# Kernel optimization log

Measured on AMD Instinct MI355X. Metric: run time of the kernel, lower is better.

Reference implementation:

```python
import jax, jax.numpy as jnp
import numpy as np

N = 50000      # nodes
E = 1600000    # edges
F_IN = 128     # input_dim
H = 160        # hidden_dim
G = 512        # graphs in batch
C = 2          # num_classes
EPS = 1e-5     # BatchNorm eps


def setup_inputs() -> dict:
    key = jax.random.key(0)
    ks = jax.random.split(key, 12)
    x = jax.random.normal(ks[0], (N, F_IN), jnp.float32)
    edge_index = jax.random.randint(ks[1], (2, E), 0, N, dtype=jnp.int32)
    batch = jnp.sort(jax.random.randint(ks[2], (N,), 0, G, dtype=jnp.int32))

    def lin(k, fi, fo):
        s = 1.0 / np.sqrt(fi)
        kw, kb = jax.random.split(k)
        W = jax.random.uniform(kw, (fi, fo), jnp.float32, -s, s)
        b = jax.random.uniform(kb, (fo,), jnp.float32, -s, s)
        return W, b

    W1, b1 = lin(ks[3], F_IN, H)
    W2, b2 = lin(ks[4], H, H)
    W3, b3 = lin(ks[5], H, H)
    Wc1, bc1 = lin(ks[6], H, H // 2)
    Wc2, bc2 = lin(ks[7], H // 2, C)

    def bn(k):
        k1, k2, k3, k4 = jax.random.split(k, 4)
        gamma = jax.random.uniform(k1, (H,), jnp.float32, 0.5, 1.5)
        beta = jax.random.normal(k2, (H,), jnp.float32) * 0.1
        mean = jax.random.normal(k3, (H,), jnp.float32) * 0.1
        var = jax.random.uniform(k4, (H,), jnp.float32, 0.5, 1.5)
        return gamma, beta, mean, var

    g1, be1, m1, v1 = bn(ks[8])
    g2, be2, m2, v2 = bn(ks[9])
    g3, be3, m3, v3 = bn(ks[10])

    return dict(x=x, edge_index=edge_index, batch=batch,
                W1=W1, b1=b1, W2=W2, b2=b2, W3=W3, b3=b3,
                g1=g1, be1=be1, m1=m1, v1=v1,
                g2=g2, be2=be2, m2=m2, v2=v2,
                g3=g3, be3=be3, m3=m3, v3=v3,
                Wc1=Wc1, bc1=bc1, Wc2=Wc2, bc2=bc2)


def gcn_conv(x, W, b, src, dst):
    """PyG GCNConv: symmetric deg normalization with self-loops; lin -> aggregate -> +bias."""
    n = x.shape[0]
    h = x @ W                                   # [N, H]
    loop = jnp.arange(n, dtype=src.dtype)
    s = jnp.concatenate([src, loop])            # self-loops appended
    d = jnp.concatenate([dst, loop])
    deg = jax.ops.segment_sum(jnp.ones_like(d, jnp.float32), d, num_segments=n)
    inv = jnp.where(deg > 0, jax.lax.rsqrt(deg), 0.0)
    msg = h[s] * (inv[s] * inv[d])[:, None]     # [E+N, H] gather + norm
    return jax.ops.segment_sum(msg, d, num_segments=n) + b


def bn_eval(x, gamma, beta, mean, var):
    return (x - mean) * jax.lax.rsqrt(var + EPS) * gamma + beta


def reference(x, edge_index, batch, W1, b1, W2, b2, W3, b3,
              g1, be1, m1, v1, g2, be2, m2, v2, g3, be3, m3, v3,
              Wc1, bc1, Wc2, bc2):
    src, dst = edge_index[0], edge_index[1]
    # eval mode: dropout is identity, BN uses running stats
    h = jax.nn.relu(bn_eval(gcn_conv(x, W1, b1, src, dst), g1, be1, m1, v1))
    h = jax.nn.relu(bn_eval(gcn_conv(h, W2, b2, src, dst), g2, be2, m2, v2))
    h = jax.nn.relu(bn_eval(gcn_conv(h, W3, b3, src, dst), g3, be3, m3, v3))
    # global mean pool over graph ids
    sums = jax.ops.segment_sum(h, batch, num_segments=G)
    cnt = jax.ops.segment_sum(jnp.ones((h.shape[0],), jnp.float32), batch, num_segments=G)
    pooled = sums / jnp.clip(cnt, 1.0)[:, None]
    # MLP head
    z = jax.nn.relu(pooled @ Wc1 + bc1)
    return z @ Wc2 + bc2
```

## Files before the change

### kernel.cpp

```cpp
#include <hip/hip_runtime.h>

#define N_NODES   50000
#define N_EDGES   1600000
#define FDIM_IN   128
#define HDIM      160
#define N_GRAPHS  512
#define BN_EPS    1e-5f
#define NBKT_MAX  128

typedef short  frag8 __attribute__((ext_vector_type(8)));
typedef float  facc4 __attribute__((ext_vector_type(4)));


__device__ __forceinline__ unsigned short f2bf(float f) {
    unsigned int u = __float_as_uint(f);
    return (unsigned short)((u + 0x7FFFu + ((u >> 16) & 1u)) >> 16);
}

__device__ __forceinline__ unsigned int pack2(float lo, float hi) {
    return (unsigned int)f2bf(lo) | ((unsigned int)f2bf(hi) << 16);
}

__device__ __forceinline__ void addpk(float* acc, uint4 r) {
    acc[0] += __uint_as_float(r.x << 16);
    acc[1] += __uint_as_float(r.x & 0xFFFF0000u);
    acc[2] += __uint_as_float(r.y << 16);
    acc[3] += __uint_as_float(r.y & 0xFFFF0000u);
    acc[4] += __uint_as_float(r.z << 16);
    acc[5] += __uint_as_float(r.z & 0xFFFF0000u);
    acc[6] += __uint_as_float(r.w << 16);
    acc[7] += __uint_as_float(r.w & 0xFFFF0000u);
}


__global__ __launch_bounds__(256) void coarse_hist_kernel(const int* __restrict__ dst,
                                                          int* __restrict__ cg, int E) {
    __shared__ int h[NBKT_MAX];
    int tid = threadIdx.x;
    if (tid < NBKT_MAX) h[tid] = 0;
    __syncthreads();
    for (int e = blockIdx.x * 256 + tid; e < E; e += gridDim.x * 256)
        atomicAdd(&h[dst[e] >> 9], 1);
    __syncthreads();
    if (tid < NBKT_MAX && h[tid]) atomicAdd(&cg[tid], h[tid]);
}

__global__ __launch_bounds__(128) void coarse_scan_kernel(const int* __restrict__ cg,
                                                          int* __restrict__ bucket_base,
                                                          int* __restrict__ bucket_cursor) {
    __shared__ int h[NBKT_MAX];
    int t = threadIdx.x;
    h[t] = cg[t];
    __syncthreads();
    if (t == 0) {
        int run = 0;
        for (int i = 0; i < NBKT_MAX; ++i) { int c = h[i]; h[i] = run; run += c; }
    }
    __syncthreads();
    bucket_base[t] = h[t];
    bucket_cursor[t] = h[t];
    if (t == 0) bucket_base[NBKT_MAX] = h[NBKT_MAX - 1] + cg[NBKT_MAX - 1];
}

__global__ __launch_bounds__(256) void part_kernel(const int* __restrict__ src,
                                                   const int* __restrict__ dst,
                                                   int* __restrict__ bucket_cursor,
                                                   unsigned int* __restrict__ pairs, int E) {
    __shared__ int bcnt[NBKT_MAX], bbase[NBKT_MAX], lc[NBKT_MAX];
    int tid = threadIdx.x;
    int per = (E + gridDim.x - 1) / gridDim.x;
    int beg = blockIdx.x * per;
    int end = min(beg + per, E);
    if (tid < NBKT_MAX) { bcnt[tid] = 0; lc[tid] = 0; }
    __syncthreads();
    for (int e = beg + tid; e < end; e += 256)
        atomicAdd(&bcnt[dst[e] >> 9], 1);
    __syncthreads();
    if (tid < NBKT_MAX)
        bbase[tid] = bcnt[tid] ? atomicAdd(&bucket_cursor[tid], bcnt[tid]) : 0;
    __syncthreads();
    for (int e = beg + tid; e < end; e += 256) {
        int d = dst[e];
        int b = d >> 9;
        int pos = bbase[b] + atomicAdd(&lc[b], 1);
        pairs[pos] = ((unsigned int)src[e] << 9) | (unsigned int)(d & 511);
    }
}

__global__ __launch_bounds__(1024) void bucket_csr_kernel(const unsigned int* __restrict__ pairs,
                                                          const int* __restrict__ bucket_base,
                                                          int* __restrict__ row_off,
                                                          float* __restrict__ inv,
                                                          int* __restrict__ ssrc, int n) {
    __shared__ int h[512];
    __shared__ int ws[8];
    int tid = threadIdx.x;
    int b = blockIdx.x;
    int node0 = b << 9;
    int beg = bucket_base[b], end = bucket_base[b + 1];
    if (tid < 512) h[tid] = 0;
    __syncthreads();
    for (int j = beg + tid; j < end; j += 1024)
        atomicAdd(&h[pairs[j] & 511], 1);
    __syncthreads();
    int cntv = (tid < 512) ? h[tid] : 0;
    __syncthreads();
    int lane = tid & 63, wid = tid >> 6;
    int incl = cntv;
    #pragma unroll
    for (int off = 1; off < 64; off <<= 1) {
        int u = __shfl_up(incl, off);
        if (lane >= off) incl += u;
    }
    if (tid < 512 && lane == 63) ws[wid] = incl;
    __syncthreads();
    if (tid == 0) {
        int r = 0;
        #pragma unroll
        for (int i = 0; i < 8; ++i) { int t = ws[i]; ws[i] = r; r += t; }
    }
    __syncthreads();
    int excl = (tid < 512) ? (ws[wid] + incl - cntv) : 0;
    if (tid < 512) {
        int node = node0 + tid;
        if (node < n) {
            row_off[node] = beg + excl;
            inv[node] = rsqrtf((float)(cntv + 1));
        }
        h[tid] = excl;
    }
    if (tid == 0 && (node0 + 512) >= n) row_off[n] = end;
    __syncthreads();
    for (int j = beg + tid; j < end; j += 1024) {
        unsigned int p = pairs[j];
        int pos = beg + atomicAdd(&h[p & 511], 1);
        ssrc[pos] = (int)(p >> 9);
    }
}


__global__ void prep_kernel(const float* __restrict__ b, const float* __restrict__ g,
                            const float* __restrict__ be, const float* __restrict__ m,
                            const float* __restrict__ v, float* __restrict__ sc,
                            float* __restrict__ sh) {
    int t = threadIdx.x;
    if (t < HDIM) {
        float s = g[t] * rsqrtf(v[t] + BN_EPS);
        sc[t] = s;
        sh[t] = (b[t] - m[t]) * s + be[t];
    }
}


template <int K>
__global__ __launch_bounds__(256) void pack_w_kernel(const float* __restrict__ W,
                                                     unsigned short* __restrict__ out) {
    int tid = blockIdx.x * 256 + threadIdx.x;
    if (tid >= K * 160) return;
    int j = tid & 7;
    int l = (tid >> 3) & 63;
    int u = (tid >> 9) % 10;
    int t = tid / 5120;
    int k = t * 32 + (l >> 4) * 8 + j;
    int nn = u * 16 + (l & 15);
    out[tid] = f2bf(W[k * 160 + nn]);
}


__global__ __launch_bounds__(256) void scale_bf16_kernel(const float* __restrict__ x,
                                                         const float* __restrict__ inv,
                                                         unsigned short* __restrict__ out,
                                                         int n) {
    int i = blockIdx.x * 256 + threadIdx.x;
    if (i < n * 32) {
        int node = i >> 5;
        float w = inv[node];
        float4 v = ((const float4*)x)[i];
        ushort4 o;
        o.x = f2bf(v.x * w); o.y = f2bf(v.y * w);
        o.z = f2bf(v.z * w); o.w = f2bf(v.w * w);
        ((ushort4*)out)[i] = o;
    }
}


template <int C>
__global__ __launch_bounds__(256) void agg_grp_kernel(const unsigned short* __restrict__ in_s,
                                                      const float* __restrict__ inv,
                                                      const int* __restrict__ row_off,
                                                      const int* __restrict__ ssrc,
                                                      unsigned short* __restrict__ out, int n) {
    constexpr int LPR = C / 8;
    constexpr int G   = 64 / LPR;
    constexpr int RB  = C * 2;
    int wave = threadIdx.x >> 6;
    int lane = threadIdx.x & 63;
    int node = blockIdx.x * 4 + wave;
    if (node >= n) return;
    int g  = lane / LPR;
    int cl = lane - g * LPR;
    bool act = g < G;
    int beg = row_off[node], end = row_off[node + 1];
    const char* base = (const char*)in_s;
    int lb = cl * 16;

    float acc[8];
    #pragma unroll
    for (int i = 0; i < 8; ++i) acc[i] = 0.f;

    if (g == 0) {
        uint4 r = *(const uint4*)(base + (size_t)node * RB + lb);
        addpk(acc, r);
    }

    int e = act ? beg + g : end;
    for (; e + G < end; e += 2 * G) {
        int s0 = ssrc[e], s1 = ssrc[e + G];
        uint4 r0 = *(const uint4*)(base + (size_t)s0 * RB + lb);
        uint4 r1 = *(const uint4*)(base + (size_t)s1 * RB + lb);
        addpk(acc, r0);
        addpk(acc, r1);
    }
    if (e < end) {
        uint4 r = *(const uint4*)(base + (size_t)ssrc[e] * RB + lb);
        addpk(acc, r);
    }

    if (G == 4) {
        #pragma unroll
        for (int i = 0; i < 8; ++i) acc[i] += __shfl(acc[i], lane + 32);
        #pragma unroll
        for (int i = 0; i < 8; ++i) acc[i] += __shfl(acc[i], lane + 16);
    } else {
        #pragma unroll
        for (int i = 0; i < 8; ++i) {
            float a = __shfl(acc[i], lane + 20);
            float b = __shfl(acc[i], lane + 40);
            acc[i] += a + b;
        }
    }

    if (lane < LPR) {
        float wi = inv[node];
        uint4 o;
        o.x = pack2(acc[0] * wi, acc[1] * wi);
        o.y = pack2(acc[2] * wi, acc[3] * wi);
        o.z = pack2(acc[4] * wi, acc[5] * wi);
        o.w = pack2(acc[6] * wi, acc[7] * wi);
        *(uint4*)((char*)out + (size_t)node * RB + lb) = o;
    }
}


template <int K, int OUTMODE>
__global__ __launch_bounds__(256) void mfma_gemm_kernel(const unsigned short* __restrict__ A,
                                                        const unsigned short* __restrict__ Bp,
                                                        const float* __restrict__ sc,
                                                        const float* __restrict__ sh,
                                                        const float* __restrict__ inv,
                                                        float* __restrict__ CoutF,
                                                        unsigned short* __restrict__ CoutB,
                                                        int n) {
    constexpr int KT = K / 32;
    int tid = threadIdx.x;
    int wave = tid >> 6, lane = tid & 63;
    int row0 = blockIdx.x * 64 + wave * 16;
    int m = lane & 15, q = lane >> 4;

    int arow = row0 + m;
    int arowc = (arow < n) ? arow : (n - 1);
    const frag8* Abase = (const frag8*)(A + (size_t)arowc * K);
    const frag8* Bbase = (const frag8*)Bp;

    facc4 acc[10];
    #pragma unroll
    for (int u = 0; u < 10; ++u) acc[u] = (facc4){0.f, 0.f, 0.f, 0.f};

    #pragma unroll
    for (int t = 0; t < KT; ++t) {
        frag8 af = Abase[t * 4 + q];
        #pragma unroll
        for (int u = 0; u < 10; ++u) {
            frag8 bf = Bbase[(t * 10 + u) * 64 + lane];
            acc[u] = __builtin_amdgcn_mfma_f32_16x16x32_bf16(af, bf, acc[u], 0, 0, 0);
        }
    }

    #pragma unroll
    for (int u = 0; u < 10; ++u) {
        int c = u * 16 + m;
        float scv = sc[c], shv = sh[c];
        #pragma unroll
        for (int r = 0; r < 4; ++r) {
            int rr = row0 + q * 4 + r;
            if (rr < n) {
                float v = fmaxf(acc[u][r] * scv + shv, 0.f);
                if (OUTMODE == 1) {
                    CoutB[(size_t)rr * 160 + c] = f2bf(v * inv[rr]);
                } else {
                    CoutF[(size_t)rr * 160 + c] = v;
                }
            }
        }
    }
}


__global__ __launch_bounds__(256) void pool_head_kernel(const float* __restrict__ h,
                                                        const int* __restrict__ batch,
                                                        const float* __restrict__ Wc1,
                                                        const float* __restrict__ bc1,
                                                        const float* __restrict__ Wc2,
                                                        const float* __restrict__ bc2,
                                                        float* __restrict__ out, int n) {
    __shared__ float pooled[160];
    __shared__ float z[80];
    __shared__ int range[2];
    int g = blockIdx.x;
    int t = threadIdx.x;
    if (t < 2) {
        int target = g + t;
        int lo = 0, hi = n;
        while (lo < hi) {
            int mid = (lo + hi) >> 1;
            if (batch[mid] < target) lo = mid + 1; else hi = mid;
        }
        range[t] = lo;
    }
    __syncthreads();
    int lo = range[0], hi = range[1];
    if (t < 160) {
        float s = 0.f;
        for (int r = lo; r < hi; ++r) s += h[(size_t)r * 160 + t];
        pooled[t] = s / fmaxf((float)(hi - lo), 1.f);
    }
    __syncthreads();
    if (t < 80) {
        float s = bc1[t];
        for (int k = 0; k < 160; ++k) s += pooled[k] * Wc1[k * 80 + t];
        z[t] = fmaxf(s, 0.f);
    }
    __syncthreads();
    if (t < 2) {
        float s = bc2[t];
        for (int k = 0; k < 80; ++k) s += z[k] * Wc2[k * 2 + t];
        out[g * 2 + t] = s;
    }
}


static inline size_t align256(size_t x) { return (x + 255) & ~(size_t)255; }

extern "C" void kernel_launch(void* const* d_in, const int* in_sizes, int n_in,
                              void* d_out, int out_size, void* d_ws, size_t ws_size,
                              hipStream_t stream) {
    const float* x   = (const float*)d_in[0];
    const int* ei    = (const int*)d_in[1];
    const int* batch = (const int*)d_in[2];
    const float* W1  = (const float*)d_in[3];
    const float* b1  = (const float*)d_in[4];
    const float* W2  = (const float*)d_in[5];
    const float* b2  = (const float*)d_in[6];
    const float* W3  = (const float*)d_in[7];
    const float* b3  = (const float*)d_in[8];
    const float* g1  = (const float*)d_in[9];
    const float* be1 = (const float*)d_in[10];
    const float* m1  = (const float*)d_in[11];
    const float* v1  = (const float*)d_in[12];
    const float* g2  = (const float*)d_in[13];
    const float* be2 = (const float*)d_in[14];
    const float* m2  = (const float*)d_in[15];
    const float* v2  = (const float*)d_in[16];
    const float* g3  = (const float*)d_in[17];
    const float* be3 = (const float*)d_in[18];
    const float* m3  = (const float*)d_in[19];
    const float* v3  = (const float*)d_in[20];
    const float* Wc1 = (const float*)d_in[21];
    const float* bc1 = (const float*)d_in[22];
    const float* Wc2 = (const float*)d_in[23];
    const float* bc2 = (const float*)d_in[24];
    float* out = (float*)d_out;

    const int N = in_sizes[2];
    const int E = in_sizes[1] / 2;
    const int* src = ei;
    const int* dst = ei + E;

    char* w = (char*)d_ws;
    int*   row_off = (int*)w;             w += align256((size_t)(N + 1) * 4);
    float* inv     = (float*)w;           w += align256((size_t)N * 4);
    int*   ssrc    = (int*)w;             w += align256((size_t)E * 4);
    unsigned int* pairs = (unsigned int*)w; w += align256((size_t)E * 4);
    int*   cg      = (int*)w;             w += align256((size_t)NBKT_MAX * 4);
    int*   bucket_base   = (int*)w;       w += align256((size_t)(NBKT_MAX + 1) * 4);
    int*   bucket_cursor = (int*)w;       w += align256((size_t)NBKT_MAX * 4);
    float* scsh    = (float*)w;           w += align256((size_t)6 * HDIM * 4);
    unsigned short* W1p = (unsigned short*)w;  w += align256((size_t)FDIM_IN * HDIM * 2);
    unsigned short* W2p = (unsigned short*)w;  w += align256((size_t)HDIM * HDIM * 2);
    unsigned short* W3p = (unsigned short*)w;  w += align256((size_t)HDIM * HDIM * 2);
    unsigned short* bufA_bf = (unsigned short*)w;  w += align256((size_t)N * HDIM * 2);
    char* regionR = w;
    unsigned short* xs_bf = (unsigned short*)regionR;
    unsigned short* hs_bf = (unsigned short*)(regionR + align256((size_t)N * FDIM_IN * 2));
    float* bufB = (float*)regionR;
    float* sc1 = scsh, *sh1 = scsh + 160, *sc2 = scsh + 320, *sh2 = scsh + 480,
         * sc3 = scsh + 640, *sh3 = scsh + 800;

    hipMemsetAsync(cg, 0, (size_t)NBKT_MAX * 4, stream);

    coarse_hist_kernel<<<256, 256, 0, stream>>>(dst, cg, E);
    coarse_scan_kernel<<<1, 128, 0, stream>>>(cg, bucket_base, bucket_cursor);
    part_kernel<<<256, 256, 0, stream>>>(src, dst, bucket_cursor, pairs, E);
    int nbkt = (N + 511) >> 9;
    bucket_csr_kernel<<<nbkt, 1024, 0, stream>>>(pairs, bucket_base, row_off, inv, ssrc, N);

    prep_kernel<<<1, 256, 0, stream>>>(b1, g1, be1, m1, v1, sc1, sh1);
    prep_kernel<<<1, 256, 0, stream>>>(b2, g2, be2, m2, v2, sc2, sh2);
    prep_kernel<<<1, 256, 0, stream>>>(b3, g3, be3, m3, v3, sc3, sh3);
    pack_w_kernel<128><<<(128 * 160 + 255) / 256, 256, 0, stream>>>(W1, W1p);
    pack_w_kernel<160><<<(160 * 160 + 255) / 256, 256, 0, stream>>>(W2, W2p);
    pack_w_kernel<160><<<(160 * 160 + 255) / 256, 256, 0, stream>>>(W3, W3p);

    int gAgg = (N + 3) / 4;
    int gGemm = (N + 63) / 64;

    scale_bf16_kernel<<<(N * 32 + 255) / 256, 256, 0, stream>>>(x, inv, xs_bf, N);
    agg_grp_kernel<128><<<gAgg, 256, 0, stream>>>(xs_bf, inv, row_off, ssrc, bufA_bf, N);
    mfma_gemm_kernel<128, 1><<<gGemm, 256, 0, stream>>>(bufA_bf, W1p, sc1, sh1, inv, nullptr, hs_bf, N);
    agg_grp_kernel<160><<<gAgg, 256, 0, stream>>>(hs_bf, inv, row_off, ssrc, bufA_bf, N);
    mfma_gemm_kernel<160, 1><<<gGemm, 256, 0, stream>>>(bufA_bf, W2p, sc2, sh2, inv, nullptr, hs_bf, N);
    agg_grp_kernel<160><<<gAgg, 256, 0, stream>>>(hs_bf, inv, row_off, ssrc, bufA_bf, N);
    mfma_gemm_kernel<160, 0><<<gGemm, 256, 0, stream>>>(bufA_bf, W3p, sc3, sh3, inv, bufB, nullptr, N);

    pool_head_kernel<<<N_GRAPHS, 256, 0, stream>>>(bufB, batch, Wc1, bc1, Wc2, bc2, out, N);
}
```

Measured before the change: 476.1 us.

## Split features into eight column slabs and shrink source indices to 16 bits

Node feature tables are stored as eight column slabs (16 or 20 bf16 per node per slab), and each aggregation block handles one slab, so a slab's gather working set is small enough to stay cache-resident. The GEMM epilogue and the scaling kernel now write this slab layout. CSR source indices are stored as unsigned short to halve index traffic. The cost is eight passes over the edge list per layer (index reads multiplied), narrower 8-byte gathers, and more shuffle reductions. The 16-bit indices only hold because N = 50000 is below 65536.

Result: slower. 633.9 us (+33.1%).

```diff
diff --git a/kernel.cpp b/kernel.cpp
--- a/kernel.cpp
+++ b/kernel.cpp
@@ -21,15 +21,11 @@
     return (unsigned int)f2bf(lo) | ((unsigned int)f2bf(hi) << 16);
 }
 
-__device__ __forceinline__ void addpk(float* acc, uint4 r) {
+__device__ __forceinline__ void addpk4(float* acc, uint2 r) {
     acc[0] += __uint_as_float(r.x << 16);
     acc[1] += __uint_as_float(r.x & 0xFFFF0000u);
     acc[2] += __uint_as_float(r.y << 16);
     acc[3] += __uint_as_float(r.y & 0xFFFF0000u);
-    acc[4] += __uint_as_float(r.z << 16);
-    acc[5] += __uint_as_float(r.z & 0xFFFF0000u);
-    acc[6] += __uint_as_float(r.w << 16);
-    acc[7] += __uint_as_float(r.w & 0xFFFF0000u);
 }
 
 
@@ -91,7 +87,7 @@
                                                           const int* __restrict__ bucket_base,
                                                           int* __restrict__ row_off,
                                                           float* __restrict__ inv,
-                                                          int* __restrict__ ssrc, int n) {
+                                                          unsigned short* __restrict__ ssrc, int n) {
     __shared__ int h[512];
     __shared__ int ws[8];
     int tid = threadIdx.x;
@@ -134,7 +130,7 @@
     for (int j = beg + tid; j < end; j += 1024) {
         unsigned int p = pairs[j];
         int pos = beg + atomicAdd(&h[p & 511], 1);
-        ssrc[pos] = (int)(p >> 9);
+        ssrc[pos] = (unsigned short)(p >> 9);
     }
 }
 
@@ -167,87 +163,95 @@
 }
 
 
-__global__ __launch_bounds__(256) void scale_bf16_kernel(const float* __restrict__ x,
+__global__ __launch_bounds__(256) void scale_slab_kernel(const float* __restrict__ x,
                                                          const float* __restrict__ inv,
-                                                         unsigned short* __restrict__ out,
+                                                         unsigned short* __restrict__ slabs,
                                                          int n) {
     int i = blockIdx.x * 256 + threadIdx.x;
     if (i < n * 32) {
         int node = i >> 5;
+        int f = i & 31;
+        int s = f >> 2;
+        int o = f & 3;
         float w = inv[node];
         float4 v = ((const float4*)x)[i];
-        ushort4 o;
-        o.x = f2bf(v.x * w); o.y = f2bf(v.y * w);
-        o.z = f2bf(v.z * w); o.w = f2bf(v.w * w);
-        ((ushort4*)out)[i] = o;
+        ushort4 ov;
+        ov.x = f2bf(v.x * w); ov.y = f2bf(v.y * w);
+        ov.z = f2bf(v.z * w); ov.w = f2bf(v.w * w);
+        *(ushort4*)(slabs + (size_t)s * n * 16 + (size_t)node * 16 + o * 4) = ov;
     }
 }
 
 
 template <int C>
-__global__ __launch_bounds__(256) void agg_grp_kernel(const unsigned short* __restrict__ in_s,
-                                                      const float* __restrict__ inv,
-                                                      const int* __restrict__ row_off,
-                                                      const int* __restrict__ ssrc,
-                                                      unsigned short* __restrict__ out, int n) {
-    constexpr int LPR = C / 8;
-    constexpr int G   = 64 / LPR;
-    constexpr int RB  = C * 2;
+__global__ __launch_bounds__(256) void agg_slab_kernel(const unsigned short* __restrict__ slabs,
+                                                       const float* __restrict__ inv,
+                                                       const int* __restrict__ row_off,
+                                                       const unsigned short* __restrict__ ssrc,
+                                                       unsigned short* __restrict__ out, int n) {
+    constexpr int SLICE = C / 8;
+    constexpr int LPE   = SLICE / 4;
+    constexpr int G     = 64 / LPE;
+    constexpr int NPW   = 4;
     int wave = threadIdx.x >> 6;
     int lane = threadIdx.x & 63;
-    int node = blockIdx.x * 4 + wave;
-    if (node >= n) return;
-    int g  = lane / LPR;
-    int cl = lane - g * LPR;
-    bool act = g < G;
-    int beg = row_off[node], end = row_off[node + 1];
-    const char* base = (const char*)in_s;
-    int lb = cl * 16;
-
-    float acc[8];
-    #pragma unroll
-    for (int i = 0; i < 8; ++i) acc[i] = 0.f;
-
-    if (g == 0) {
-        uint4 r = *(const uint4*)(base + (size_t)node * RB + lb);
-        addpk(acc, r);
-    }
-
-    int e = act ? beg + g : end;
-    for (; e + G < end; e += 2 * G) {
-        int s0 = ssrc[e], s1 = ssrc[e + G];
-        uint4 r0 = *(const uint4*)(base + (size_t)s0 * RB + lb);
-        uint4 r1 = *(const uint4*)(base + (size_t)s1 * RB + lb);
-        addpk(acc, r0);
-        addpk(acc, r1);
-    }
-    if (e < end) {
-        uint4 r = *(const uint4*)(base + (size_t)ssrc[e] * RB + lb);
-        addpk(acc, r);
-    }
-
-    if (G == 4) {
-        #pragma unroll
-        for (int i = 0; i < 8; ++i) acc[i] += __shfl(acc[i], lane + 32);
-        #pragma unroll
-        for (int i = 0; i < 8; ++i) acc[i] += __shfl(acc[i], lane + 16);
-    } else {
-        #pragma unroll
-        for (int i = 0; i < 8; ++i) {
-            float a = __shfl(acc[i], lane + 20);
-            float b = __shfl(acc[i], lane + 40);
-            acc[i] += a + b;
+    int x  = blockIdx.x & 7;
+    int nb = blockIdx.x >> 3;
+    const uint2* slab = (const uint2*)(slabs + (size_t)x * n * SLICE);
+    int g  = lane / LPE;
+    int cl = lane - g * LPE;
+    bool act = (LPE * G == 64) ? true : (g < G);
+
+    for (int k = 0; k < NPW; ++k) {
+        int node = nb * (4 * NPW) + k * 4 + wave;
+        if (node < n) {
+            int beg = row_off[node], end = row_off[node + 1];
+            float acc[4] = {0.f, 0.f, 0.f, 0.f};
+            if (g == 0) {
+                uint2 r = slab[(size_t)node * LPE + cl];
+                addpk4(acc, r);
+            }
+            int e = act ? beg + g : end;
+            for (; e + G < end; e += 2 * G) {
+                int s0 = ssrc[e], s1 = ssrc[e + G];
+                uint2 r0 = slab[(size_t)s0 * LPE + cl];
+                uint2 r1 = slab[(size_t)s1 * LPE + cl];
+                addpk4(acc, r0);
+                addpk4(acc, r1);
+            }
+            if (e < end) {
+                uint2 r = slab[(size_t)ssrc[e] * LPE + cl];
+                addpk4(acc, r);
+            }
+            if (G == 16) {
+                #pragma unroll
+                for (int i = 0; i < 4; ++i) acc[i] += __shfl(acc[i], lane + 32);
+                #pragma unroll
+                for (int i = 0; i < 4; ++i) acc[i] += __shfl(acc[i], lane + 16);
+                #pragma unroll
+                for (int i = 0; i < 4; ++i) acc[i] += __shfl(acc[i], lane + 8);
+                #pragma unroll
+                for (int i = 0; i < 4; ++i) acc[i] += __shfl(acc[i], lane + 4);
+            } else {
+                #pragma unroll
+                for (int i = 0; i < 4; ++i) acc[i] += __shfl(acc[i], lane + 30);
+                #pragma unroll
+                for (int i = 0; i < 4; ++i) acc[i] += __shfl(acc[i], lane + 15);
+                #pragma unroll
+                for (int i = 0; i < 4; ++i) {
+                    float a = __shfl(acc[i], lane + 5);
+                    float b = __shfl(acc[i], lane + 10);
+                    acc[i] += a + b;
+                }
+            }
+            if (lane < LPE) {
+                float wi = inv[node];
+                uint2 o;
+                o.x = pack2(acc[0] * wi, acc[1] * wi);
+                o.y = pack2(acc[2] * wi, acc[3] * wi);
+                *(uint2*)(out + (size_t)node * C + x * SLICE + cl * 4) = o;
+            }
         }
-    }
-
-    if (lane < LPR) {
-        float wi = inv[node];
-        uint4 o;
-        o.x = pack2(acc[0] * wi, acc[1] * wi);
-        o.y = pack2(acc[2] * wi, acc[3] * wi);
-        o.z = pack2(acc[4] * wi, acc[5] * wi);
-        o.w = pack2(acc[6] * wi, acc[7] * wi);
-        *(uint4*)((char*)out + (size_t)node * RB + lb) = o;
     }
 }
 
@@ -290,13 +294,14 @@
     for (int u = 0; u < 10; ++u) {
         int c = u * 16 + m;
         float scv = sc[c], shv = sh[c];
+        int s = c / 20, o = c - s * 20;
         #pragma unroll
         for (int r = 0; r < 4; ++r) {
             int rr = row0 + q * 4 + r;
             if (rr < n) {
                 float v = fmaxf(acc[u][r] * scv + shv, 0.f);
                 if (OUTMODE == 1) {
-                    CoutB[(size_t)rr * 160 + c] = f2bf(v * inv[rr]);
+                    CoutB[(size_t)s * n * 20 + (size_t)rr * 20 + o] = f2bf(v * inv[rr]);
                 } else {
                     CoutF[(size_t)rr * 160 + c] = v;
                 }
@@ -389,7 +394,7 @@
     char* w = (char*)d_ws;
     int*   row_off = (int*)w;             w += align256((size_t)(N + 1) * 4);
     float* inv     = (float*)w;           w += align256((size_t)N * 4);
-    int*   ssrc    = (int*)w;             w += align256((size_t)E * 4);
+    unsigned short* ssrc = (unsigned short*)w; w += align256((size_t)E * 2);
     unsigned int* pairs = (unsigned int*)w; w += align256((size_t)E * 4);
     int*   cg      = (int*)w;             w += align256((size_t)NBKT_MAX * 4);
     int*   bucket_base   = (int*)w;       w += align256((size_t)(NBKT_MAX + 1) * 4);
@@ -400,8 +405,8 @@
     unsigned short* W3p = (unsigned short*)w;  w += align256((size_t)HDIM * HDIM * 2);
     unsigned short* bufA_bf = (unsigned short*)w;  w += align256((size_t)N * HDIM * 2);
     char* regionR = w;
-    unsigned short* xs_bf = (unsigned short*)regionR;
-    unsigned short* hs_bf = (unsigned short*)(regionR + align256((size_t)N * FDIM_IN * 2));
+    unsigned short* xs_sl = (unsigned short*)regionR;
+    unsigned short* hs_sl = (unsigned short*)(regionR + align256((size_t)N * FDIM_IN * 2));
     float* bufB = (float*)regionR;
     float* sc1 = scsh, *sh1 = scsh + 160, *sc2 = scsh + 320, *sh2 = scsh + 480,
          * sc3 = scsh + 640, *sh3 = scsh + 800;
@@ -421,15 +426,15 @@
     pack_w_kernel<160><<<(160 * 160 + 255) / 256, 256, 0, stream>>>(W2, W2p);
     pack_w_kernel<160><<<(160 * 160 + 255) / 256, 256, 0, stream>>>(W3, W3p);
 
-    int gAgg = (N + 3) / 4;
+    int gAgg = ((N + 15) / 16) * 8;
     int gGemm = (N + 63) / 64;
 
-    scale_bf16_kernel<<<(N * 32 + 255) / 256, 256, 0, stream>>>(x, inv, xs_bf, N);
-    agg_grp_kernel<128><<<gAgg, 256, 0, stream>>>(xs_bf, inv, row_off, ssrc, bufA_bf, N);
-    mfma_gemm_kernel<128, 1><<<gGemm, 256, 0, stream>>>(bufA_bf, W1p, sc1, sh1, inv, nullptr, hs_bf, N);
-    agg_grp_kernel<160><<<gAgg, 256, 0, stream>>>(hs_bf, inv, row_off, ssrc, bufA_bf, N);
-    mfma_gemm_kernel<160, 1><<<gGemm, 256, 0, stream>>>(bufA_bf, W2p, sc2, sh2, inv, nullptr, hs_bf, N);
-    agg_grp_kernel<160><<<gAgg, 256, 0, stream>>>(hs_bf, inv, row_off, ssrc, bufA_bf, N);
+    scale_slab_kernel<<<(N * 32 + 255) / 256, 256, 0, stream>>>(x, inv, xs_sl, N);
+    agg_slab_kernel<128><<<gAgg, 256, 0, stream>>>(xs_sl, inv, row_off, ssrc, bufA_bf, N);
+    mfma_gemm_kernel<128, 1><<<gGemm, 256, 0, stream>>>(bufA_bf, W1p, sc1, sh1, inv, nullptr, hs_sl, N);
+    agg_slab_kernel<160><<<gAgg, 256, 0, stream>>>(hs_sl, inv, row_off, ssrc, bufA_bf, N);
+    mfma_gemm_kernel<160, 1><<<gGemm, 256, 0, stream>>>(bufA_bf, W2p, sc2, sh2, inv, nullptr, hs_sl, N);
+    agg_slab_kernel<160><<<gAgg, 256, 0, stream>>>(hs_sl, inv, row_off, ssrc, bufA_bf, N);
     mfma_gemm_kernel<160, 0><<<gGemm, 256, 0, stream>>>(bufA_bf, W3p, sc3, sh3, inv, bufB, nullptr, N);
 
     pool_head_kernel<<<N_GRAPHS, 256, 0, stream>>>(bufB, batch, Wc1, bc1, Wc2, bc2, out, N);
```

## Sort neighbor lists by source range, use 16-bit indices, batch nodes per wave

Applied to the files above, without the earlier changes.

The CSR build now counting-sorts each destination row's edges into 16 source sub-ranges of 4096 nodes, so neighbors within a row are grouped by source region. Source indices are stored as 16-bit values, halving index traffic, which works because the node count fits in 16 bits. The aggregation kernel now processes 8 nodes per wave in a loop instead of one, which cuts block count and launch overhead. The cost is a larger shared-memory histogram and scan in the CSR kernel (8192 bins), and the 16-bit indices cap node count at 65536.

Result: no change. 485.4 us (+1.9%).

```diff
diff --git a/kernel.cpp b/kernel.cpp
--- a/kernel.cpp
+++ b/kernel.cpp
@@ -21,7 +21,7 @@
     return (unsigned int)f2bf(lo) | ((unsigned int)f2bf(hi) << 16);
 }
 
-__device__ __forceinline__ void addpk(float* acc, uint4 r) {
+__device__ __forceinline__ void addpk8(float* acc, uint4 r) {
     acc[0] += __uint_as_float(r.x << 16);
     acc[1] += __uint_as_float(r.x & 0xFFFF0000u);
     acc[2] += __uint_as_float(r.y << 16);
@@ -91,50 +91,64 @@
                                                           const int* __restrict__ bucket_base,
                                                           int* __restrict__ row_off,
                                                           float* __restrict__ inv,
-                                                          int* __restrict__ ssrc, int n) {
-    __shared__ int h[512];
-    __shared__ int ws[8];
+                                                          unsigned short* __restrict__ ssrc, int n) {
+    __shared__ int h[8192];
+    __shared__ int ts[1024];
+    __shared__ int ws[16];
     int tid = threadIdx.x;
     int b = blockIdx.x;
     int node0 = b << 9;
     int beg = bucket_base[b], end = bucket_base[b + 1];
-    if (tid < 512) h[tid] = 0;
-    __syncthreads();
-    for (int j = beg + tid; j < end; j += 1024)
-        atomicAdd(&h[pairs[j] & 511], 1);
-    __syncthreads();
-    int cntv = (tid < 512) ? h[tid] : 0;
-    __syncthreads();
+    for (int i = tid; i < 8192; i += 1024) h[i] = 0;
+    __syncthreads();
+    for (int j = beg + tid; j < end; j += 1024) {
+        unsigned int p = pairs[j];
+        int dl = p & 511;
+        int sb = (p >> 9) >> 12;
+        atomicAdd(&h[dl * 16 + sb], 1);
+    }
+    __syncthreads();
+    int base8 = tid * 8;
+    int s = 0;
+    #pragma unroll
+    for (int i = 0; i < 8; ++i) s += h[base8 + i];
+    ts[tid] = s;
     int lane = tid & 63, wid = tid >> 6;
-    int incl = cntv;
+    int incl = s;
     #pragma unroll
     for (int off = 1; off < 64; off <<= 1) {
         int u = __shfl_up(incl, off);
         if (lane >= off) incl += u;
     }
-    if (tid < 512 && lane == 63) ws[wid] = incl;
+    if (lane == 63) ws[wid] = incl;
     __syncthreads();
     if (tid == 0) {
         int r = 0;
         #pragma unroll
-        for (int i = 0; i < 8; ++i) { int t = ws[i]; ws[i] = r; r += t; }
-    }
-    __syncthreads();
-    int excl = (tid < 512) ? (ws[wid] + incl - cntv) : 0;
+        for (int i = 0; i < 16; ++i) { int t = ws[i]; ws[i] = r; r += t; }
+    }
+    __syncthreads();
+    int run = ws[wid] + incl - s;
+    #pragma unroll
+    for (int i = 0; i < 8; ++i) { int c = h[base8 + i]; h[base8 + i] = run; run += c; }
+    __syncthreads();
     if (tid < 512) {
         int node = node0 + tid;
         if (node < n) {
-            row_off[node] = beg + excl;
-            inv[node] = rsqrtf((float)(cntv + 1));
-        }
-        h[tid] = excl;
+            row_off[node] = beg + h[tid * 16];
+            int cnt = ts[2 * tid] + ts[2 * tid + 1];
+            inv[node] = rsqrtf((float)(cnt + 1));
+        }
     }
     if (tid == 0 && (node0 + 512) >= n) row_off[n] = end;
     __syncthreads();
     for (int j = beg + tid; j < end; j += 1024) {
         unsigned int p = pairs[j];
-        int pos = beg + atomicAdd(&h[p & 511], 1);
-        ssrc[pos] = (int)(p >> 9);
+        int dl = p & 511;
+        int src = (int)(p >> 9);
+        int sb = src >> 12;
+        int pos = beg + atomicAdd(&h[dl * 16 + sb], 1);
+        ssrc[pos] = (unsigned short)src;
     }
 }
 
@@ -185,69 +199,65 @@
 
 
 template <int C>
-__global__ __launch_bounds__(256) void agg_grp_kernel(const unsigned short* __restrict__ in_s,
-                                                      const float* __restrict__ inv,
-                                                      const int* __restrict__ row_off,
-                                                      const int* __restrict__ ssrc,
-                                                      unsigned short* __restrict__ out, int n) {
+__global__ __launch_bounds__(256) void agg_sorted_kernel(const unsigned short* __restrict__ in_s,
+                                                         const float* __restrict__ inv,
+                                                         const int* __restrict__ row_off,
+                                                         const unsigned short* __restrict__ ssrc,
+                                                         unsigned short* __restrict__ out, int n) {
     constexpr int LPR = C / 8;
     constexpr int G   = 64 / LPR;
-    constexpr int RB  = C * 2;
+    constexpr int NPW = 8;
     int wave = threadIdx.x >> 6;
     int lane = threadIdx.x & 63;
-    int node = blockIdx.x * 4 + wave;
-    if (node >= n) return;
     int g  = lane / LPR;
     int cl = lane - g * LPR;
-    bool act = g < G;
-    int beg = row_off[node], end = row_off[node + 1];
-    const char* base = (const char*)in_s;
-    int lb = cl * 16;
-
-    float acc[8];
-    #pragma unroll
-    for (int i = 0; i < 8; ++i) acc[i] = 0.f;
-
-    if (g == 0) {
-        uint4 r = *(const uint4*)(base + (size_t)node * RB + lb);
-        addpk(acc, r);
-    }
-
-    int e = act ? beg + g : end;
-    for (; e + G < end; e += 2 * G) {
-        int s0 = ssrc[e], s1 = ssrc[e + G];
-        uint4 r0 = *(const uint4*)(base + (size_t)s0 * RB + lb);
-        uint4 r1 = *(const uint4*)(base + (size_t)s1 * RB + lb);
-        addpk(acc, r0);
-        addpk(acc, r1);
-    }
-    if (e < end) {
-        uint4 r = *(const uint4*)(base + (size_t)ssrc[e] * RB + lb);
-        addpk(acc, r);
-    }
-
-    if (G == 4) {
-        #pragma unroll
-        for (int i = 0; i < 8; ++i) acc[i] += __shfl(acc[i], lane + 32);
-        #pragma unroll
-        for (int i = 0; i < 8; ++i) acc[i] += __shfl(acc[i], lane + 16);
-    } else {
-        #pragma unroll
-        for (int i = 0; i < 8; ++i) {
-            float a = __shfl(acc[i], lane + 20);
-            float b = __shfl(acc[i], lane + 40);
-            acc[i] += a + b;
-        }
-    }
-
-    if (lane < LPR) {
-        float wi = inv[node];
-        uint4 o;
-        o.x = pack2(acc[0] * wi, acc[1] * wi);
-        o.y = pack2(acc[2] * wi, acc[3] * wi);
-        o.z = pack2(acc[4] * wi, acc[5] * wi);
-        o.w = pack2(acc[6] * wi, acc[7] * wi);
-        *(uint4*)((char*)out + (size_t)node * RB + lb) = o;
+    bool act = (LPR * G == 64) ? true : (g < G);
+    const uint4* base = (const uint4*)in_s;
+    int nodeBase = blockIdx.x * (4 * NPW) + wave * NPW;
+
+    for (int k = 0; k < NPW; ++k) {
+        int node = nodeBase + k;
+        if (node >= n) break;
+        int beg = row_off[node], end = row_off[node + 1];
+        float acc[8] = {0.f, 0.f, 0.f, 0.f, 0.f, 0.f, 0.f, 0.f};
+        if (g == 0) {
+            uint4 r = base[(size_t)node * LPR + cl];
+            addpk8(acc, r);
+        }
+        int e = act ? beg + g : end;
+        for (; e + G < end; e += 2 * G) {
+            int s0 = ssrc[e], s1 = ssrc[e + G];
+            uint4 r0 = base[(size_t)s0 * LPR + cl];
+            uint4 r1 = base[(size_t)s1 * LPR + cl];
+            addpk8(acc, r0);
+            addpk8(acc, r1);
+        }
+        if (e < end) {
+            uint4 r = base[(size_t)ssrc[e] * LPR + cl];
+            addpk8(acc, r);
+        }
+        if (G == 4) {
+            #pragma unroll
+            for (int i = 0; i < 8; ++i) acc[i] += __shfl(acc[i], lane + 32);
+            #pragma unroll
+            for (int i = 0; i < 8; ++i) acc[i] += __shfl(acc[i], lane + 16);
+        } else {
+            #pragma unroll
+            for (int i = 0; i < 8; ++i) {
+                float a = __shfl(acc[i], lane + 20);
+                float b = __shfl(acc[i], lane + 40);
+                acc[i] += a + b;
+            }
+        }
+        if (lane < LPR) {
+            float wi = inv[node];
+            uint4 o;
+            o.x = pack2(acc[0] * wi, acc[1] * wi);
+            o.y = pack2(acc[2] * wi, acc[3] * wi);
+            o.z = pack2(acc[4] * wi, acc[5] * wi);
+            o.w = pack2(acc[6] * wi, acc[7] * wi);
+            *(uint4*)(out + (size_t)node * C + cl * 8) = o;
+        }
     }
 }
 
@@ -389,7 +399,7 @@
     char* w = (char*)d_ws;
     int*   row_off = (int*)w;             w += align256((size_t)(N + 1) * 4);
     float* inv     = (float*)w;           w += align256((size_t)N * 4);
-    int*   ssrc    = (int*)w;             w += align256((size_t)E * 4);
+    unsigned short* ssrc = (unsigned short*)w; w += align256((size_t)E * 2);
     unsigned int* pairs = (unsigned int*)w; w += align256((size_t)E * 4);
     int*   cg      = (int*)w;             w += align256((size_t)NBKT_MAX * 4);
     int*   bucket_base   = (int*)w;       w += align256((size_t)(NBKT_MAX + 1) * 4);
@@ -421,15 +431,15 @@
     pack_w_kernel<160><<<(160 * 160 + 255) / 256, 256, 0, stream>>>(W2, W2p);
     pack_w_kernel<160><<<(160 * 160 + 255) / 256, 256, 0, stream>>>(W3, W3p);
 
-    int gAgg = (N + 3) / 4;
+    int gAgg = (N + 31) / 32;
     int gGemm = (N + 63) / 64;
 
     scale_bf16_kernel<<<(N * 32 + 255) / 256, 256, 0, stream>>>(x, inv, xs_bf, N);
-    agg_grp_kernel<128><<<gAgg, 256, 0, stream>>>(xs_bf, inv, row_off, ssrc, bufA_bf, N);
+    agg_sorted_kernel<128><<<gAgg, 256, 0, stream>>>(xs_bf, inv, row_off, ssrc, bufA_bf, N);
     mfma_gemm_kernel<128, 1><<<gGemm, 256, 0, stream>>>(bufA_bf, W1p, sc1, sh1, inv, nullptr, hs_bf, N);
-    agg_grp_kernel<160><<<gAgg, 256, 0, stream>>>(hs_bf, inv, row_off, ssrc, bufA_bf, N);
+    agg_sorted_kernel<160><<<gAgg, 256, 0, stream>>>(hs_bf, inv, row_off, ssrc, bufA_bf, N);
     mfma_gemm_kernel<160, 1><<<gGemm, 256, 0, stream>>>(bufA_bf, W2p, sc2, sh2, inv, nullptr, hs_bf, N);
-    agg_grp_kernel<160><<<gAgg, 256, 0, stream>>>(hs_bf, inv, row_off, ssrc, bufA_bf, N);
+    agg_sorted_kernel<160><<<gAgg, 256, 0, stream>>>(hs_bf, inv, row_off, ssrc, bufA_bf, N);
     mfma_gemm_kernel<160, 0><<<gGemm, 256, 0, stream>>>(bufA_bf, W3p, sc3, sh3, inv, bufB, nullptr, N);
 
     pool_head_kernel<<<N_GRAPHS, 256, 0, stream>>>(bufB, batch, Wc1, bc1, Wc2, bc2, out, N);
```
